# Performance work log

Hardware: AMD Instinct MI355X
Metric: run time of the kernel (lower is better)

## Reference

```python
import jax, jax.numpy as jnp
import numpy as np


def rational_hat(points, centers, radius):
    # points: [B, P, 2], centers: [K, 2], radius: [1]
    # L1 distance of each point to each center: [B, P, K]
    norm = jnp.abs(points[:, :, None, :] - centers[None, None, :, :]).sum(-1)
    r = jnp.abs(radius[0])
    val = 1.0 / (1.0 + norm) - 1.0 / (1.0 + jnp.abs(r - norm))
    return val.sum(axis=1)  # [B, K]


def setup_inputs() -> dict:
    key = jax.random.key(0)
    k1, k2, k3, k4, k5 = jax.random.split(key, 5)
    B, N0, N1, N2, K = 32, 20000, 10000, 10000, 64
    return {
        "beta_0_up": jax.random.uniform(k1, (B, N0, 2), dtype=jnp.float32),
        "beta_0_down": jax.random.uniform(k2, (B, N0, 2), dtype=jnp.float32),
        "beta0_ext": jax.random.uniform(k3, (B, N1, 2), dtype=jnp.float32),
        "beta1_ext": jax.random.uniform(k4, (B, N2, 2), dtype=jnp.float32),
        "centers": jax.random.uniform(k5, (K, 2), dtype=jnp.float32),
        "radius": jnp.full((1,), 0.1, dtype=jnp.float32),
    }


def reference(beta_0_up, beta_0_down, beta0_ext, beta1_ext, centers, radius):
    x0, y0 = beta0_ext[..., 0], beta0_ext[..., 1]
    x1, y1 = beta1_ext[..., 0], beta1_ext[..., 1]
    b0_1st = jnp.stack([x0, 1.0 - x0], axis=-1)  # [B, N1, 2]
    b0_2nd = jnp.stack([y0, 1.0 - y0], axis=-1)
    b1_1st = jnp.stack([x1, 1.0 - x1], axis=-1)  # [B, N2, 2]
    b1_2nd = jnp.stack([y1, 1.0 - y1], axis=-1)
    ph_down = jnp.concatenate([beta_0_down, b0_1st, b1_1st], axis=1)  # [B, P, 2]
    ph_up = jnp.concatenate([beta_0_up, b0_2nd, b1_2nd], axis=1)
    up_out = rational_hat(ph_up, centers, radius)    # [B, K]
    down_out = rational_hat(ph_down, centers, radius)
    tpl = -((up_out - down_out) ** 2).sum()
    x = jnp.concatenate([up_out, down_out], axis=1)  # [B, 2K]
    return (x, tpl)
```

## Files before the change

### kernel.cpp

```cpp
#include <hip/hip_runtime.h>

typedef float v2f __attribute__((ext_vector_type(2)));

#define NB 32
#define N0 20000
#define N1 10000
#define N2 10000
#define NF4_A 10000
#define NF4_E0 5000
#define NF4_E 10000
#define NCH 157
#define T_A 14
#define KC_A 8
#define KC_B 16
#define NBINS 4096
#define SENT 3.0e4f

__global__ __launch_bounds__(256, 8) void hat_kernel(
    const float* __restrict__ up0, const float* __restrict__ down0,
    const float* __restrict__ ext0, const float* __restrict__ ext1,
    const float* __restrict__ centers, const float* __restrict__ radius,
    float* __restrict__ out)
{
    const int tid  = threadIdx.x;
    const int lane = tid & 63;
    const int wave = tid >> 6;
    const float r  = fabsf(radius[0]);
    const int slot = blockIdx.x;

    __shared__ unsigned hist[NBINS];
    __shared__ float    red[4 * KC_B];

    if (slot < 256) {
        const int id   = slot;
        const int cc   = id & 3;
        const int side = (id >> 2) & 1;
        const int b    = id >> 3;
        const int cbase = cc * KC_B;

        for (int j = tid; j < NBINS; j += 256) hist[j] = 0;
        __syncthreads();

        const float4* e0 = (const float4*)(ext0 + (size_t)b * (N1*2));
        const float4* e1 = (const float4*)(ext1 + (size_t)b * (N2*2));
        #define EPTR(I) ((I) < NF4_E0 ? (e0 + (I)) : (e1 + ((I) - NF4_E0)))
        float4 q = *EPTR(tid);
        for (int i = tid; i < NF4_E; i += 256) {
            const float4 qc = q;
            q = *EPTR(min(i + 256, NF4_E - 1));
            const float vv0 = (side == 0) ? qc.y : qc.x;
            const float vv1 = (side == 0) ? qc.w : qc.z;
            int b0 = (int)(vv0 * (float)NBINS);
            int b1 = (int)(vv1 * (float)NBINS);
            b0 = min(max(b0, 0), NBINS - 1);
            b1 = min(max(b1, 0), NBINS - 1);
            atomicAdd(&hist[b0], 1u);
            atomicAdd(&hist[b1], 1u);
        }
        #undef EPTR
        __syncthreads();

        float Ak[KC_B], mk[KC_B];
        #pragma unroll
        for (int k = 0; k < KC_B; ++k) {
            const float cx = centers[2*(cbase+k)];
            const float cy = centers[2*(cbase+k)+1];
            Ak[k] = fabsf(1.0f - (cx + cy));
            mk[k] = 0.5f * (1.0f + (cx - cy));
        }

        float part[KC_B];
        #pragma unroll
        for (int k = 0; k < KC_B; ++k) part[k] = 0.f;

        #pragma unroll
        for (int jj = 0; jj < NBINS/256; ++jj) {
            const int j = jj*256 + tid;
            const float cntf = (float)hist[j];
            const float vvj  = ((float)j + 0.5f) * (1.0f/(float)NBINS);
            #pragma unroll
            for (int k = 0; k < KC_B; ++k) {
                const float s  = vvj - mk[k];
                const float tt = fmaxf(Ak[k], 2.0f*fabsf(s));
                const float d1 = 1.0f + tt;
                const float rn = r - tt;
                const float d2 = 1.0f + fabsf(rn);
                const float rc = __builtin_amdgcn_rcpf(d1 * d2);
                part[k] = fmaf(cntf * (d2 - d1), rc, part[k]);
            }
        }

        {
            #pragma unroll
            for (int k = 0; k < 8; ++k) {
                const bool hi = lane & 32;
                const float send = hi ? part[k]   : part[k+8];
                const float keep = hi ? part[k+8] : part[k];
                part[k] = keep + __shfl_xor(send, 32, 64);
            }
            #pragma unroll
            for (int k = 0; k < 4; ++k) {
                const bool hi = lane & 16;
                const float send = hi ? part[k]   : part[k+4];
                const float keep = hi ? part[k+4] : part[k];
                part[k] = keep + __shfl_xor(send, 16, 64);
            }
            #pragma unroll
            for (int k = 0; k < 2; ++k) {
                const bool hi = lane & 8;
                const float send = hi ? part[k]   : part[k+2];
                const float keep = hi ? part[k+2] : part[k];
                part[k] = keep + __shfl_xor(send, 8, 64);
            }
            {
                const bool hi = lane & 4;
                const float send = hi ? part[0] : part[1];
                const float keep = hi ? part[1] : part[0];
                part[0] = keep + __shfl_xor(send, 4, 64);
            }
            part[0] += __shfl_xor(part[0], 2, 64);
            part[0] += __shfl_xor(part[0], 1, 64);
        }
        if ((lane & 3) == 0) red[wave * KC_B + (lane >> 2)] = part[0];
        __syncthreads();
        if (tid < KC_B) {
            const float s = red[tid] + red[KC_B + tid] + red[2*KC_B + tid] + red[3*KC_B + tid];
            atomicAdd(&out[b*128 + side*64 + cbase + tid], s);
        }
        return;
    }

    const int aid    = slot - 256;
    const int tchunk = aid % T_A;
    const int rest   = aid / T_A;
    const int half   = rest & 1;
    const int side   = (rest >> 1) & 1;
    const int b      = rest >> 2;
    const int cbase  = (half * 4 + wave) * KC_A;
    const int outBase = b*128 + side*64 + cbase;

    v2f nuc[KC_A], nvc[KC_A];
    #pragma unroll
    for (int k = 0; k < KC_A; ++k) {
        const float cx = centers[2*(cbase+k)];
        const float cy = centers[2*(cbase+k)+1];
        nuc[k] = (v2f){-(cx + cy), -(cx + cy)};
        nvc[k] = (v2f){-(cx - cy), -(cx - cy)};
    }

    const float4* base0 = (const float4*)((side == 0 ? up0 : down0) + (size_t)b * (N0*2));

    v2f acc[KC_A];
    #pragma unroll
    for (int k = 0; k < KC_A; ++k) acc[k] = (v2f){0.f, 0.f};
    const v2f one2 = (v2f){1.f, 1.f};

    float4 q = base0[min(tchunk*64 + lane, NF4_A - 1)];
    for (int t = tchunk; t < NCH; t += T_A) {
        const float4 qc = q;
        const int tn = t + T_A;
        if (tn < NCH) {
            q = base0[min(tn*64 + lane, NF4_A - 1)];
        }

        v2f u_ = (v2f){qc.x + qc.y, qc.z + qc.w};
        v2f v_ = (v2f){qc.x - qc.y, qc.z - qc.w};
        if (t*64 + 63 >= NF4_A) {
            const bool bad = (t*64 + lane) >= NF4_A;
            u_.x = bad ? SENT : u_.x;  u_.y = bad ? SENT : u_.y;
            v_.x = bad ? 0.f  : v_.x;  v_.y = bad ? 0.f  : v_.y;
        }

        #pragma unroll
        for (int k = 0; k < KC_A; ++k) {
            const v2f du = u_ + nuc[k];
            const v2f dv = v_ + nvc[k];
            const float tt0 = fmaxf(fabsf(du.x), fabsf(dv.x));
            const float tt1 = fmaxf(fabsf(du.y), fabsf(dv.y));
            const v2f tt = (v2f){tt0, tt1};
            const v2f d1 = tt + one2;
            const float rn0 = r - tt0;
            const float rn1 = r - tt1;
            const v2f d2 = (v2f){1.f + fabsf(rn0), 1.f + fabsf(rn1)};
            const v2f dd  = d1 * d2;
            const v2f num = d2 - d1;
            const v2f rc  = (v2f){__builtin_amdgcn_rcpf(dd.x),
                                  __builtin_amdgcn_rcpf(dd.y)};
            acc[k] = __builtin_elementwise_fma(num, rc, acc[k]);
        }
    }

    float a1[KC_A];
    #pragma unroll
    for (int k = 0; k < KC_A; ++k) a1[k] = acc[k].x + acc[k].y;

    {
        #pragma unroll
        for (int k = 0; k < 4; ++k) {
            const bool hi = lane & 32;
            const float send = hi ? a1[k]   : a1[k+4];
            const float keep = hi ? a1[k+4] : a1[k];
            a1[k] = keep + __shfl_xor(send, 32, 64);
        }
        #pragma unroll
        for (int k = 0; k < 2; ++k) {
            const bool hi = lane & 16;
            const float send = hi ? a1[k]   : a1[k+2];
            const float keep = hi ? a1[k+2] : a1[k];
            a1[k] = keep + __shfl_xor(send, 16, 64);
        }
        {
            const bool hi = lane & 8;
            const float send = hi ? a1[0] : a1[1];
            const float keep = hi ? a1[1] : a1[0];
            a1[0] = keep + __shfl_xor(send, 8, 64);
        }
        a1[0] += __shfl_xor(a1[0], 4, 64);
        a1[0] += __shfl_xor(a1[0], 2, 64);
        a1[0] += __shfl_xor(a1[0], 1, 64);
    }
    if ((lane & 7) == 0) {
        atomicAdd(&out[outBase + (lane >> 3)], a1[0]);
    }
}

__global__ __launch_bounds__(256) void tpl_kernel(float* __restrict__ out)
{
    __shared__ float red[256];
    float s = 0.f;
    for (int i = threadIdx.x; i < NB*64; i += 256) {
        const int b = i >> 6, k = i & 63;
        const float d = out[b*128 + k] - out[b*128 + 64 + k];
        s = fmaf(d, d, s);
    }
    red[threadIdx.x] = s;
    __syncthreads();
    for (int w = 128; w > 0; w >>= 1) {
        if (threadIdx.x < w) red[threadIdx.x] += red[threadIdx.x + w];
        __syncthreads();
    }
    if (threadIdx.x == 0) out[NB*128] = -red[0];
}

extern "C" void kernel_launch(void* const* d_in, const int* in_sizes, int n_in,
                              void* d_out, int out_size, void* d_ws, size_t ws_size,
                              hipStream_t stream) {
    const float* up0     = (const float*)d_in[0];
    const float* down0   = (const float*)d_in[1];
    const float* ext0    = (const float*)d_in[2];
    const float* ext1    = (const float*)d_in[3];
    const float* centers = (const float*)d_in[4];
    const float* radius  = (const float*)d_in[5];
    float* out = (float*)d_out;

    hipMemsetAsync(out, 0, NB * 128 * sizeof(float), stream);

    hat_kernel<<<dim3(256 + 1792), dim3(256), 0, stream>>>(
        up0, down0, ext0, ext1, centers, radius, out);
    tpl_kernel<<<1, 256, 0, stream>>>(out);
}
```

Measured before the change: 109.5 us.

## Fuse final reduction into main kernel via last-block counter and regrid to 512-thread blocks

Removes the separate tpl_kernel launch. Each block now bumps an atomic counter stored in the tpl output slot, and the last block to finish computes the squared-difference sum over the per-batch results. The grid is also reshaped from 2048 blocks of 256 threads to 512 blocks of 512 threads. The direct-point path now covers all 64 centers per block (8 waves) with 4 chunk slices instead of 14, so each block does more work and there are fewer blocks. The intent is to save a kernel launch and per-block overhead. The cost is a serialized tail reduction in one block and coarser load balancing across CUs.

```diff
diff --git a/kernel.cpp b/kernel.cpp
--- a/kernel.cpp
+++ b/kernel.cpp
@@ -10,13 +10,14 @@
 #define NF4_E0 5000
 #define NF4_E 10000
 #define NCH 157
-#define T_A 14
+#define T_A 4
 #define KC_A 8
 #define KC_B 16
 #define NBINS 4096
+#define NBLK 512
 #define SENT 3.0e4f
 
-__global__ __launch_bounds__(256, 8) void hat_kernel(
+__global__ __launch_bounds__(512, 4) void hat_kernel(
     const float* __restrict__ up0, const float* __restrict__ down0,
     const float* __restrict__ ext0, const float* __restrict__ ext1,
     const float* __restrict__ centers, const float* __restrict__ radius,
@@ -29,7 +30,8 @@
     const int slot = blockIdx.x;
 
     __shared__ unsigned hist[NBINS];
-    __shared__ float    red[4 * KC_B];
+    __shared__ float    red[8 * KC_B];
+    __shared__ unsigned lastFlag;
 
     if (slot < 256) {
         const int id   = slot;
@@ -38,16 +40,16 @@
         const int b    = id >> 3;
         const int cbase = cc * KC_B;
 
-        for (int j = tid; j < NBINS; j += 256) hist[j] = 0;
+        for (int j = tid; j < NBINS; j += 512) hist[j] = 0;
         __syncthreads();
 
         const float4* e0 = (const float4*)(ext0 + (size_t)b * (N1*2));
         const float4* e1 = (const float4*)(ext1 + (size_t)b * (N2*2));
         #define EPTR(I) ((I) < NF4_E0 ? (e0 + (I)) : (e1 + ((I) - NF4_E0)))
         float4 q = *EPTR(tid);
-        for (int i = tid; i < NF4_E; i += 256) {
+        for (int i = tid; i < NF4_E; i += 512) {
             const float4 qc = q;
-            q = *EPTR(min(i + 256, NF4_E - 1));
+            q = *EPTR(min(i + 512, NF4_E - 1));
             const float vv0 = (side == 0) ? qc.y : qc.x;
             const float vv1 = (side == 0) ? qc.w : qc.z;
             int b0 = (int)(vv0 * (float)NBINS);
@@ -74,8 +76,8 @@
         for (int k = 0; k < KC_B; ++k) part[k] = 0.f;
 
         #pragma unroll
-        for (int jj = 0; jj < NBINS/256; ++jj) {
-            const int j = jj*256 + tid;
+        for (int jj = 0; jj < NBINS/512; ++jj) {
+            const int j = jj*512 + tid;
             const float cntf = (float)hist[j];
             const float vvj  = ((float)j + 0.5f) * (1.0f/(float)NBINS);
             #pragma unroll
@@ -124,122 +126,130 @@
         if ((lane & 3) == 0) red[wave * KC_B + (lane >> 2)] = part[0];
         __syncthreads();
         if (tid < KC_B) {
-            const float s = red[tid] + red[KC_B + tid] + red[2*KC_B + tid] + red[3*KC_B + tid];
+            float s = 0.f;
+            #pragma unroll
+            for (int w2 = 0; w2 < 8; ++w2) s += red[w2 * KC_B + tid];
             atomicAdd(&out[b*128 + side*64 + cbase + tid], s);
         }
-        return;
+    } else {
+        const int aid    = slot - 256;
+        const int tchunk = aid & 3;
+        const int side   = (aid >> 2) & 1;
+        const int b      = aid >> 3;
+        const int cbase  = wave * KC_A;
+        const int outBase = b*128 + side*64 + cbase;
+
+        v2f nuc[KC_A], nvc[KC_A];
+        #pragma unroll
+        for (int k = 0; k < KC_A; ++k) {
+            const float cx = centers[2*(cbase+k)];
+            const float cy = centers[2*(cbase+k)+1];
+            nuc[k] = (v2f){-(cx + cy), -(cx + cy)};
+            nvc[k] = (v2f){-(cx - cy), -(cx - cy)};
+        }
+
+        const float4* base0 = (const float4*)((side == 0 ? up0 : down0) + (size_t)b * (N0*2));
+
+        v2f acc[KC_A];
+        #pragma unroll
+        for (int k = 0; k < KC_A; ++k) acc[k] = (v2f){0.f, 0.f};
+        const v2f one2 = (v2f){1.f, 1.f};
+
+        float4 q = base0[min(tchunk*64 + lane, NF4_A - 1)];
+        for (int t = tchunk; t < NCH; t += T_A) {
+            const float4 qc = q;
+            const int tn = t + T_A;
+            if (tn < NCH) {
+                q = base0[min(tn*64 + lane, NF4_A - 1)];
+            }
+
+            v2f u_ = (v2f){qc.x + qc.y, qc.z + qc.w};
+            v2f v_ = (v2f){qc.x - qc.y, qc.z - qc.w};
+            if (t*64 + 63 >= NF4_A) {
+                const bool bad = (t*64 + lane) >= NF4_A;
+                u_.x = bad ? SENT : u_.x;  u_.y = bad ? SENT : u_.y;
+                v_.x = bad ? 0.f  : v_.x;  v_.y = bad ? 0.f  : v_.y;
+            }
+
+            #pragma unroll
+            for (int k = 0; k < KC_A; ++k) {
+                const v2f du = u_ + nuc[k];
+                const v2f dv = v_ + nvc[k];
+                const float tt0 = fmaxf(fabsf(du.x), fabsf(dv.x));
+                const float tt1 = fmaxf(fabsf(du.y), fabsf(dv.y));
+                const v2f tt = (v2f){tt0, tt1};
+                const v2f d1 = tt + one2;
+                const float rn0 = r - tt0;
+                const float rn1 = r - tt1;
+                const v2f d2 = (v2f){1.f + fabsf(rn0), 1.f + fabsf(rn1)};
+                const v2f dd  = d1 * d2;
+                const v2f num = d2 - d1;
+                const v2f rc  = (v2f){__builtin_amdgcn_rcpf(dd.x),
+                                      __builtin_amdgcn_rcpf(dd.y)};
+                acc[k] = __builtin_elementwise_fma(num, rc, acc[k]);
+            }
+        }
+
+        float a1[KC_A];
+        #pragma unroll
+        for (int k = 0; k < KC_A; ++k) a1[k] = acc[k].x + acc[k].y;
+
+        {
+            #pragma unroll
+            for (int k = 0; k < 4; ++k) {
+                const bool hi = lane & 32;
+                const float send = hi ? a1[k]   : a1[k+4];
+                const float keep = hi ? a1[k+4] : a1[k];
+                a1[k] = keep + __shfl_xor(send, 32, 64);
+            }
+            #pragma unroll
+            for (int k = 0; k < 2; ++k) {
+                const bool hi = lane & 16;
+                const float send = hi ? a1[k]   : a1[k+2];
+                const float keep = hi ? a1[k+2] : a1[k];
+                a1[k] = keep + __shfl_xor(send, 16, 64);
+            }
+            {
+                const bool hi = lane & 8;
+                const float send = hi ? a1[0] : a1[1];
+                const float keep = hi ? a1[1] : a1[0];
+                a1[0] = keep + __shfl_xor(send, 8, 64);
+            }
+            a1[0] += __shfl_xor(a1[0], 4, 64);
+            a1[0] += __shfl_xor(a1[0], 2, 64);
+            a1[0] += __shfl_xor(a1[0], 1, 64);
+        }
+        if ((lane & 7) == 0) {
+            atomicAdd(&out[outBase + (lane >> 3)], a1[0]);
+        }
     }
 
-    const int aid    = slot - 256;
-    const int tchunk = aid % T_A;
-    const int rest   = aid / T_A;
-    const int half   = rest & 1;
-    const int side   = (rest >> 1) & 1;
-    const int b      = rest >> 2;
-    const int cbase  = (half * 4 + wave) * KC_A;
-    const int outBase = b*128 + side*64 + cbase;
-
-    v2f nuc[KC_A], nvc[KC_A];
-    #pragma unroll
-    for (int k = 0; k < KC_A; ++k) {
-        const float cx = centers[2*(cbase+k)];
-        const float cy = centers[2*(cbase+k)+1];
-        nuc[k] = (v2f){-(cx + cy), -(cx + cy)};
-        nvc[k] = (v2f){-(cx - cy), -(cx - cy)};
+    __syncthreads();
+    if (tid == 0) {
+        __threadfence();
+        const unsigned old = atomicAdd((unsigned*)&out[NB*128], 1u);
+        lastFlag = (old == NBLK - 1) ? 1u : 0u;
     }
-
-    const float4* base0 = (const float4*)((side == 0 ? up0 : down0) + (size_t)b * (N0*2));
-
-    v2f acc[KC_A];
-    #pragma unroll
-    for (int k = 0; k < KC_A; ++k) acc[k] = (v2f){0.f, 0.f};
-    const v2f one2 = (v2f){1.f, 1.f};
-
-    float4 q = base0[min(tchunk*64 + lane, NF4_A - 1)];
-    for (int t = tchunk; t < NCH; t += T_A) {
-        const float4 qc = q;
-        const int tn = t + T_A;
-        if (tn < NCH) {
-            q = base0[min(tn*64 + lane, NF4_A - 1)];
-        }
-
-        v2f u_ = (v2f){qc.x + qc.y, qc.z + qc.w};
-        v2f v_ = (v2f){qc.x - qc.y, qc.z - qc.w};
-        if (t*64 + 63 >= NF4_A) {
-            const bool bad = (t*64 + lane) >= NF4_A;
-            u_.x = bad ? SENT : u_.x;  u_.y = bad ? SENT : u_.y;
-            v_.x = bad ? 0.f  : v_.x;  v_.y = bad ? 0.f  : v_.y;
-        }
-
-        #pragma unroll
-        for (int k = 0; k < KC_A; ++k) {
-            const v2f du = u_ + nuc[k];
-            const v2f dv = v_ + nvc[k];
-            const float tt0 = fmaxf(fabsf(du.x), fabsf(dv.x));
-            const float tt1 = fmaxf(fabsf(du.y), fabsf(dv.y));
-            const v2f tt = (v2f){tt0, tt1};
-            const v2f d1 = tt + one2;
-            const float rn0 = r - tt0;
-            const float rn1 = r - tt1;
-            const v2f d2 = (v2f){1.f + fabsf(rn0), 1.f + fabsf(rn1)};
-            const v2f dd  = d1 * d2;
-            const v2f num = d2 - d1;
-            const v2f rc  = (v2f){__builtin_amdgcn_rcpf(dd.x),
-                                  __builtin_amdgcn_rcpf(dd.y)};
-            acc[k] = __builtin_elementwise_fma(num, rc, acc[k]);
+    __syncthreads();
+    if (lastFlag) {
+        __threadfence();
+        float s = 0.f;
+        for (int i = tid; i < NB*64; i += 512) {
+            const int b2 = i >> 6, k = i & 63;
+            const float d = out[b2*128 + k] - out[b2*128 + 64 + k];
+            s = fmaf(d, d, s);
+        }
+        #pragma unroll
+        for (int o = 32; o > 0; o >>= 1) s += __shfl_xor(s, o, 64);
+        if (lane == 0) red[wave] = s;
+        __syncthreads();
+        if (tid == 0) {
+            float t2 = 0.f;
+            #pragma unroll
+            for (int w2 = 0; w2 < 8; ++w2) t2 += red[w2];
+            out[NB*128] = -t2;
         }
     }
-
-    float a1[KC_A];
-    #pragma unroll
-    for (int k = 0; k < KC_A; ++k) a1[k] = acc[k].x + acc[k].y;
-
-    {
-        #pragma unroll
-        for (int k = 0; k < 4; ++k) {
-            const bool hi = lane & 32;
-            const float send = hi ? a1[k]   : a1[k+4];
-            const float keep = hi ? a1[k+4] : a1[k];
-            a1[k] = keep + __shfl_xor(send, 32, 64);
-        }
-        #pragma unroll
-        for (int k = 0; k < 2; ++k) {
-            const bool hi = lane & 16;
-            const float send = hi ? a1[k]   : a1[k+2];
-            const float keep = hi ? a1[k+2] : a1[k];
-            a1[k] = keep + __shfl_xor(send, 16, 64);
-        }
-        {
-            const bool hi = lane & 8;
-            const float send = hi ? a1[0] : a1[1];
-            const float keep = hi ? a1[1] : a1[0];
-            a1[0] = keep + __shfl_xor(send, 8, 64);
-        }
-        a1[0] += __shfl_xor(a1[0], 4, 64);
-        a1[0] += __shfl_xor(a1[0], 2, 64);
-        a1[0] += __shfl_xor(a1[0], 1, 64);
-    }
-    if ((lane & 7) == 0) {
-        atomicAdd(&out[outBase + (lane >> 3)], a1[0]);
-    }
-}
-
-__global__ __launch_bounds__(256) void tpl_kernel(float* __restrict__ out)
-{
-    __shared__ float red[256];
-    float s = 0.f;
-    for (int i = threadIdx.x; i < NB*64; i += 256) {
-        const int b = i >> 6, k = i & 63;
-        const float d = out[b*128 + k] - out[b*128 + 64 + k];
-        s = fmaf(d, d, s);
-    }
-    red[threadIdx.x] = s;
-    __syncthreads();
-    for (int w = 128; w > 0; w >>= 1) {
-        if (threadIdx.x < w) red[threadIdx.x] += red[threadIdx.x + w];
-        __syncthreads();
-    }
-    if (threadIdx.x == 0) out[NB*128] = -red[0];
 }
 
 extern "C" void kernel_launch(void* const* d_in, const int* in_sizes, int n_in,
@@ -253,9 +263,8 @@
     const float* radius  = (const float*)d_in[5];
     float* out = (float*)d_out;
 
-    hipMemsetAsync(out, 0, NB * 128 * sizeof(float), stream);
-
-    hat_kernel<<<dim3(256 + 1792), dim3(256), 0, stream>>>(
+    hipMemsetAsync(out, 0, (NB * 128 + 1) * sizeof(float), stream);
+
+    hat_kernel<<<dim3(NBLK), dim3(512), 0, stream>>>(
         up0, down0, ext0, ext1, centers, radius, out);
-    tpl_kernel<<<1, 256, 0, stream>>>(out);
 }
```

Measured after the change: 121.4 us. 1.11x slower.

## Fuse tpl reduction into hat kernel via last-block counter; double-buffer loads

Applied to the files above, without the earlier changes.

Removes the separate tpl_kernel launch. Each block bumps an atomic counter stored in the output slot, and the last block to finish computes the squared-difference reduction. The A-path loop also now keeps two float4 prefetches in flight and unrolls by two chunks to hide more load latency. The gain is mainly one less kernel launch. The cost is a threadfence and an atomic per block, and it relies on the output slot holding the counter as integer bits before it is overwritten with the final float.

```diff
diff --git a/kernel.cpp b/kernel.cpp
--- a/kernel.cpp
+++ b/kernel.cpp
@@ -14,6 +14,7 @@
 #define KC_A 8
 #define KC_B 16
 #define NBINS 4096
+#define NBLK 2048
 #define SENT 3.0e4f
 
 __global__ __launch_bounds__(256, 8) void hat_kernel(
@@ -30,6 +31,7 @@
 
     __shared__ unsigned hist[NBINS];
     __shared__ float    red[4 * KC_B];
+    __shared__ unsigned lastFlag;
 
     if (slot < 256) {
         const int id   = slot;
@@ -127,119 +129,128 @@
             const float s = red[tid] + red[KC_B + tid] + red[2*KC_B + tid] + red[3*KC_B + tid];
             atomicAdd(&out[b*128 + side*64 + cbase + tid], s);
         }
-        return;
+    } else {
+        const int aid    = slot - 256;
+        const int tchunk = aid % T_A;
+        const int rest   = aid / T_A;
+        const int half   = rest & 1;
+        const int side   = (rest >> 1) & 1;
+        const int b      = rest >> 2;
+        const int cbase  = (half * 4 + wave) * KC_A;
+        const int outBase = b*128 + side*64 + cbase;
+
+        v2f nuc[KC_A], nvc[KC_A];
+        #pragma unroll
+        for (int k = 0; k < KC_A; ++k) {
+            const float cx = centers[2*(cbase+k)];
+            const float cy = centers[2*(cbase+k)+1];
+            nuc[k] = (v2f){-(cx + cy), -(cx + cy)};
+            nvc[k] = (v2f){-(cx - cy), -(cx - cy)};
+        }
+
+        const float4* base0 = (const float4*)((side == 0 ? up0 : down0) + (size_t)b * (N0*2));
+
+        v2f acc[KC_A];
+        #pragma unroll
+        for (int k = 0; k < KC_A; ++k) acc[k] = (v2f){0.f, 0.f};
+        const v2f one2 = (v2f){1.f, 1.f};
+
+        #define ABODY(QC, TT) do {                                             \
+            v2f u_ = (v2f){(QC).x + (QC).y, (QC).z + (QC).w};                  \
+            v2f v_ = (v2f){(QC).x - (QC).y, (QC).z - (QC).w};                  \
+            if ((TT)*64 + 63 >= NF4_A) {             \
+                const bool bad = ((TT)*64 + lane) >= NF4_A;                    \
+                u_.x = bad ? SENT : u_.x;  u_.y = bad ? SENT : u_.y;           \
+                v_.x = bad ? 0.f  : v_.x;  v_.y = bad ? 0.f  : v_.y;           \
+            }                                                                  \
+            _Pragma("unroll")                                                  \
+            for (int k = 0; k < KC_A; ++k) {                                   \
+                const v2f du = u_ + nuc[k];                                    \
+                const v2f dv = v_ + nvc[k];                                    \
+                const float tt0 = fmaxf(fabsf(du.x), fabsf(dv.x));             \
+                const float tt1 = fmaxf(fabsf(du.y), fabsf(dv.y));             \
+                const v2f tt = (v2f){tt0, tt1};                                \
+                const v2f d1 = tt + one2;                                      \
+                const float rn0 = r - tt0;                                     \
+                const float rn1 = r - tt1;                                     \
+                const v2f d2 = (v2f){1.f + fabsf(rn0), 1.f + fabsf(rn1)};      \
+                const v2f dd  = d1 * d2;                                       \
+                const v2f num = d2 - d1;                                       \
+                const v2f rc  = (v2f){__builtin_amdgcn_rcpf(dd.x),             \
+                                      __builtin_amdgcn_rcpf(dd.y)};            \
+                acc[k] = __builtin_elementwise_fma(num, rc, acc[k]);           \
+            }                                                                  \
+        } while (0)
+
+        float4 q0 = base0[min(tchunk*64 + lane, NF4_A - 1)];
+        float4 q1 = base0[min((tchunk + T_A)*64 + lane, NF4_A - 1)];
+        for (int t = tchunk; t < NCH; t += 2*T_A) {
+            const float4 qa = q0, qb = q1;
+            const int t2 = t + 2*T_A, t3 = t + 3*T_A;
+            if (t2 < NCH) q0 = base0[min(t2*64 + lane, NF4_A - 1)];
+            if (t3 < NCH) q1 = base0[min(t3*64 + lane, NF4_A - 1)];
+            ABODY(qa, t);
+            if (t + T_A < NCH) ABODY(qb, t + T_A);
+        }
+        #undef ABODY
+
+        float a1[KC_A];
+        #pragma unroll
+        for (int k = 0; k < KC_A; ++k) a1[k] = acc[k].x + acc[k].y;
+
+        {
+            #pragma unroll
+            for (int k = 0; k < 4; ++k) {
+                const bool hi = lane & 32;
+                const float send = hi ? a1[k]   : a1[k+4];
+                const float keep = hi ? a1[k+4] : a1[k];
+                a1[k] = keep + __shfl_xor(send, 32, 64);
+            }
+            #pragma unroll
+            for (int k = 0; k < 2; ++k) {
+                const bool hi = lane & 16;
+                const float send = hi ? a1[k]   : a1[k+2];
+                const float keep = hi ? a1[k+2] : a1[k];
+                a1[k] = keep + __shfl_xor(send, 16, 64);
+            }
+            {
+                const bool hi = lane & 8;
+                const float send = hi ? a1[0] : a1[1];
+                const float keep = hi ? a1[1] : a1[0];
+                a1[0] = keep + __shfl_xor(send, 8, 64);
+            }
+            a1[0] += __shfl_xor(a1[0], 4, 64);
+            a1[0] += __shfl_xor(a1[0], 2, 64);
+            a1[0] += __shfl_xor(a1[0], 1, 64);
+        }
+        if ((lane & 7) == 0) {
+            atomicAdd(&out[outBase + (lane >> 3)], a1[0]);
+        }
     }
 
-    const int aid    = slot - 256;
-    const int tchunk = aid % T_A;
-    const int rest   = aid / T_A;
-    const int half   = rest & 1;
-    const int side   = (rest >> 1) & 1;
-    const int b      = rest >> 2;
-    const int cbase  = (half * 4 + wave) * KC_A;
-    const int outBase = b*128 + side*64 + cbase;
-
-    v2f nuc[KC_A], nvc[KC_A];
-    #pragma unroll
-    for (int k = 0; k < KC_A; ++k) {
-        const float cx = centers[2*(cbase+k)];
-        const float cy = centers[2*(cbase+k)+1];
-        nuc[k] = (v2f){-(cx + cy), -(cx + cy)};
-        nvc[k] = (v2f){-(cx - cy), -(cx - cy)};
+    __syncthreads();
+    if (tid == 0) {
+        __threadfence();
+        const unsigned old = atomicAdd((unsigned*)&out[NB*128], 1u);
+        lastFlag = (old == NBLK - 1) ? 1u : 0u;
     }
-
-    const float4* base0 = (const float4*)((side == 0 ? up0 : down0) + (size_t)b * (N0*2));
-
-    v2f acc[KC_A];
-    #pragma unroll
-    for (int k = 0; k < KC_A; ++k) acc[k] = (v2f){0.f, 0.f};
-    const v2f one2 = (v2f){1.f, 1.f};
-
-    float4 q = base0[min(tchunk*64 + lane, NF4_A - 1)];
-    for (int t = tchunk; t < NCH; t += T_A) {
-        const float4 qc = q;
-        const int tn = t + T_A;
-        if (tn < NCH) {
-            q = base0[min(tn*64 + lane, NF4_A - 1)];
-        }
-
-        v2f u_ = (v2f){qc.x + qc.y, qc.z + qc.w};
-        v2f v_ = (v2f){qc.x - qc.y, qc.z - qc.w};
-        if (t*64 + 63 >= NF4_A) {
-            const bool bad = (t*64 + lane) >= NF4_A;
-            u_.x = bad ? SENT : u_.x;  u_.y = bad ? SENT : u_.y;
-            v_.x = bad ? 0.f  : v_.x;  v_.y = bad ? 0.f  : v_.y;
-        }
-
-        #pragma unroll
-        for (int k = 0; k < KC_A; ++k) {
-            const v2f du = u_ + nuc[k];
-            const v2f dv = v_ + nvc[k];
-            const float tt0 = fmaxf(fabsf(du.x), fabsf(dv.x));
-            const float tt1 = fmaxf(fabsf(du.y), fabsf(dv.y));
-            const v2f tt = (v2f){tt0, tt1};
-            const v2f d1 = tt + one2;
-            const float rn0 = r - tt0;
-            const float rn1 = r - tt1;
-            const v2f d2 = (v2f){1.f + fabsf(rn0), 1.f + fabsf(rn1)};
-            const v2f dd  = d1 * d2;
-            const v2f num = d2 - d1;
-            const v2f rc  = (v2f){__builtin_amdgcn_rcpf(dd.x),
-                                  __builtin_amdgcn_rcpf(dd.y)};
-            acc[k] = __builtin_elementwise_fma(num, rc, acc[k]);
+    __syncthreads();
+    if (lastFlag) {
+        __threadfence();
+        float s = 0.f;
+        for (int i = tid; i < NB*64; i += 256) {
+            const int b2 = i >> 6, k = i & 63;
+            const float d = out[b2*128 + k] - out[b2*128 + 64 + k];
+            s = fmaf(d, d, s);
+        }
+        #pragma unroll
+        for (int o = 32; o > 0; o >>= 1) s += __shfl_xor(s, o, 64);
+        if (lane == 0) red[wave] = s;
+        __syncthreads();
+        if (tid == 0) {
+            out[NB*128] = -(red[0] + red[1] + red[2] + red[3]);
         }
     }
-
-    float a1[KC_A];
-    #pragma unroll
-    for (int k = 0; k < KC_A; ++k) a1[k] = acc[k].x + acc[k].y;
-
-    {
-        #pragma unroll
-        for (int k = 0; k < 4; ++k) {
-            const bool hi = lane & 32;
-            const float send = hi ? a1[k]   : a1[k+4];
-            const float keep = hi ? a1[k+4] : a1[k];
-            a1[k] = keep + __shfl_xor(send, 32, 64);
-        }
-        #pragma unroll
-        for (int k = 0; k < 2; ++k) {
-            const bool hi = lane & 16;
-            const float send = hi ? a1[k]   : a1[k+2];
-            const float keep = hi ? a1[k+2] : a1[k];
-            a1[k] = keep + __shfl_xor(send, 16, 64);
-        }
-        {
-            const bool hi = lane & 8;
-            const float send = hi ? a1[0] : a1[1];
-            const float keep = hi ? a1[1] : a1[0];
-            a1[0] = keep + __shfl_xor(send, 8, 64);
-        }
-        a1[0] += __shfl_xor(a1[0], 4, 64);
-        a1[0] += __shfl_xor(a1[0], 2, 64);
-        a1[0] += __shfl_xor(a1[0], 1, 64);
-    }
-    if ((lane & 7) == 0) {
-        atomicAdd(&out[outBase + (lane >> 3)], a1[0]);
-    }
-}
-
-__global__ __launch_bounds__(256) void tpl_kernel(float* __restrict__ out)
-{
-    __shared__ float red[256];
-    float s = 0.f;
-    for (int i = threadIdx.x; i < NB*64; i += 256) {
-        const int b = i >> 6, k = i & 63;
-        const float d = out[b*128 + k] - out[b*128 + 64 + k];
-        s = fmaf(d, d, s);
-    }
-    red[threadIdx.x] = s;
-    __syncthreads();
-    for (int w = 128; w > 0; w >>= 1) {
-        if (threadIdx.x < w) red[threadIdx.x] += red[threadIdx.x + w];
-        __syncthreads();
-    }
-    if (threadIdx.x == 0) out[NB*128] = -red[0];
 }
 
 extern "C" void kernel_launch(void* const* d_in, const int* in_sizes, int n_in,
@@ -253,9 +264,8 @@
     const float* radius  = (const float*)d_in[5];
     float* out = (float*)d_out;
 
-    hipMemsetAsync(out, 0, NB * 128 * sizeof(float), stream);
-
-    hat_kernel<<<dim3(256 + 1792), dim3(256), 0, stream>>>(
+    hipMemsetAsync(out, 0, (NB * 128 + 1) * sizeof(float), stream);
+
+    hat_kernel<<<dim3(NBLK), dim3(256), 0, stream>>>(
         up0, down0, ext0, ext1, centers, radius, out);
-    tpl_kernel<<<1, 256, 0, stream>>>(out);
 }
```

Result: slower. 184.0 us (+67.9%).
